# Performance work log

Measured on AMD Instinct MI355X. Metric: run time of the kernel, lower is better.

Reference implementation:

```python
import jax, jax.numpy as jnp
import numpy as np

B, T, D = 4, 2048, 1024
H = 16
HD = D // H  # 64


def setup_inputs() -> dict:
    key = jax.random.key(0)
    ks = jax.random.split(key, 5)
    scale = 0.02
    x = jax.random.normal(ks[0], (B, T, D), dtype=jnp.float32)
    W_qkv = jax.random.normal(ks[1], (D, 3 * D), dtype=jnp.float32) * scale
    b_qkv = jnp.zeros((3 * D,), dtype=jnp.float32)
    W_proj = jax.random.normal(ks[2], (D, D), dtype=jnp.float32) * scale
    b_proj = jnp.zeros((D,), dtype=jnp.float32)
    return {"x": x, "W_qkv": W_qkv, "b_qkv": b_qkv, "W_proj": W_proj, "b_proj": b_proj}


def reference(x, W_qkv, b_qkv, W_proj, b_proj):
    b, t, c = x.shape
    qkv = x @ W_qkv + b_qkv  # [b, t, 3c]
    q, k, v = jnp.split(qkv, 3, axis=-1)
    # [b, h, t, hd]
    q = q.reshape(b, t, H, HD).transpose(0, 2, 1, 3)
    k = k.reshape(b, t, H, HD).transpose(0, 2, 1, 3)
    v = v.reshape(b, t, H, HD).transpose(0, 2, 1, 3)
    att = jnp.einsum('bhqd,bhkd->bhqk', q, k) / jnp.sqrt(jnp.float32(HD))
    causal = jnp.tril(jnp.ones((t, t), dtype=bool))
    att = jnp.where(causal[None, None], att, jnp.float32(-jnp.inf))
    att = jax.nn.softmax(att, axis=-1)
    y = jnp.einsum('bhqk,bhkd->bhqd', att, v)
    y = y.transpose(0, 2, 1, 3).reshape(b, t, c)
    return y @ W_proj + b_proj
```

## Files before the change

kernel.cpp:

```cpp
#include <hip/hip_runtime.h>
#include <hip/hip_bf16.h>
#include <cmath>
#include <cstdint>
#include <type_traits>

#define B_ 4
#define T_ 2048
#define D_ 1024
#define H_ 16
#define HD_ 64
#define M_ (B_*T_)
#define NQKV_ 3072

#define SCALE_Q 0.18033688011112042f

typedef float f32x4 __attribute__((ext_vector_type(4)));
typedef float f32x16 __attribute__((ext_vector_type(16)));
typedef __bf16 bf16x8 __attribute__((ext_vector_type(8)));
typedef __bf16 bf16x4 __attribute__((ext_vector_type(4)));

#define MFMA16(a, b, c) __builtin_amdgcn_mfma_f32_16x16x32_bf16((a), (b), (c), 0, 0, 0)
#define MFMA32(a, b, c) __builtin_amdgcn_mfma_f32_32x32x16_bf16((a), (b), (c), 0, 0, 0)

#if defined(__has_builtin)
#if __has_builtin(__builtin_amdgcn_global_load_lds)
#define HAVE_GLDS 1
#endif
#if __has_builtin(__builtin_amdgcn_exp2f)
#define EXP2(x) __builtin_amdgcn_exp2f(x)
#endif
#endif
#ifndef EXP2
#define EXP2(x) exp2f(x)
#endif

#ifdef HAVE_GLDS
#define GLDS16(g, l) __builtin_amdgcn_global_load_lds( \
    (const __attribute__((address_space(1))) void*)(g), \
    (__attribute__((address_space(3))) void*)(l), 16, 0, 0)
#endif

__device__ inline uint32_t pack2bf(float a, float b) {
  union { __bf16 h[2]; uint32_t u; } x;
  x.h[0] = (__bf16)a; x.h[1] = (__bf16)b;
  return x.u;
}

__global__ __launch_bounds__(256) void k_cvt_bf16(const float4* __restrict__ in,
                                                  bf16x4* __restrict__ out, int n4) {
  int i = blockIdx.x * 256 + threadIdx.x;
  if (i >= n4) return;
  float4 v = in[i];
  bf16x4 o;
  o[0] = (__bf16)v.x; o[1] = (__bf16)v.y; o[2] = (__bf16)v.z; o[3] = (__bf16)v.w;
  out[i] = o;
}

__global__ __launch_bounds__(256) void k_transpose_cvt(const float* __restrict__ in,
                                                       __bf16* __restrict__ out,
                                                       int R, int C) {
  __shared__ float tile[64][65];
  int r0 = blockIdx.y * 64, c0 = blockIdx.x * 64;
#pragma unroll
  for (int i = 0; i < 16; ++i) {
    int e = threadIdx.x + i * 256;
    int lr = e >> 6, lc = e & 63;
    tile[lr][lc] = in[(size_t)(r0 + lr) * C + c0 + lc];
  }
  __syncthreads();
#pragma unroll
  for (int i = 0; i < 16; ++i) {
    int e = threadIdx.x + i * 256;
    int lc = e >> 6, lr = e & 63;
    out[(size_t)(c0 + lc) * R + r0 + lr] = (__bf16)tile[lr][lc];
  }
}

template <int MODE>
__global__ __launch_bounds__(256) void k_gemm(const __bf16* __restrict__ A,
                                              const __bf16* __restrict__ Bt,
                                              const float* __restrict__ bias,
                                              float* __restrict__ Cf,
                                              __bf16* __restrict__ Qb,
                                              __bf16* __restrict__ Kb,
                                              __bf16* __restrict__ Vtmp,
                                              int K, int N) {
  __shared__ __bf16 lA[128 * 32];
  __shared__ __bf16 lB[128 * 32];
  const int tid = threadIdx.x;
  const int lane = tid & 63, w = tid >> 6;
  const int wr = w >> 1, wc = w & 1;
  const int r15 = lane & 15, rg = lane >> 4;
  const int mb = blockIdx.y, nb = blockIdx.x;
  const int nk = K >> 5;

  const f32x4 zero = {0.f, 0.f, 0.f, 0.f};
  f32x4 acc[4][4];
#pragma unroll
  for (int m = 0; m < 4; ++m)
#pragma unroll
    for (int n = 0; n < 4; ++n) acc[m][n] = zero;

  const int c0 = tid, c1 = tid + 256;
  const int rowA0 = c0 >> 2, offA0 = (c0 & 3) * 8;
  const int rowA1 = c1 >> 2, offA1 = (c1 & 3) * 8;
  const __bf16* Ab = A + (size_t)(mb * 128) * K;
  const __bf16* Bb = Bt + (size_t)(nb * 128) * K;

  for (int kb = 0; kb < nk; ++kb) {
    __syncthreads();
#ifdef HAVE_GLDS
    GLDS16(Ab + (size_t)rowA0 * K + kb * 32 + offA0, &lA[c0 * 8]);
    GLDS16(Ab + (size_t)rowA1 * K + kb * 32 + offA1, &lA[c1 * 8]);
    GLDS16(Bb + (size_t)rowA0 * K + kb * 32 + offA0, &lB[c0 * 8]);
    GLDS16(Bb + (size_t)rowA1 * K + kb * 32 + offA1, &lB[c1 * 8]);
#else
    {
      bf16x8 ta0 = *(const bf16x8*)(Ab + (size_t)rowA0 * K + kb * 32 + offA0);
      bf16x8 ta1 = *(const bf16x8*)(Ab + (size_t)rowA1 * K + kb * 32 + offA1);
      bf16x8 tb0 = *(const bf16x8*)(Bb + (size_t)rowA0 * K + kb * 32 + offA0);
      bf16x8 tb1 = *(const bf16x8*)(Bb + (size_t)rowA1 * K + kb * 32 + offA1);
      *(bf16x8*)(&lA[c0 * 8]) = ta0;
      *(bf16x8*)(&lA[c1 * 8]) = ta1;
      *(bf16x8*)(&lB[c0 * 8]) = tb0;
      *(bf16x8*)(&lB[c1 * 8]) = tb1;
    }
#endif
    __syncthreads();
    bf16x8 af[4], bfr[4];
#pragma unroll
    for (int m = 0; m < 4; ++m)
      af[m] = *(const bf16x8*)(&lA[(wr * 64 + m * 16 + r15) * 32 + rg * 8]);
#pragma unroll
    for (int n = 0; n < 4; ++n)
      bfr[n] = *(const bf16x8*)(&lB[(wc * 64 + n * 16 + r15) * 32 + rg * 8]);
#pragma unroll
    for (int m = 0; m < 4; ++m)
#pragma unroll
      for (int n = 0; n < 4; ++n)
        acc[m][n] = MFMA16(af[m], bfr[n], acc[m][n]);
  }

  const int row0 = mb * 128 + wr * 64;
  const int col0 = nb * 128 + wc * 64;
#pragma unroll
  for (int m = 0; m < 4; ++m) {
#pragma unroll
    for (int n = 0; n < 4; ++n) {
#pragma unroll
      for (int j = 0; j < 4; ++j) {
        int r = row0 + m * 16 + rg * 4 + j;
        int c = col0 + n * 16 + r15;
        float v = acc[m][n][j] + bias[c];
        if (MODE == 0) {
          Cf[(size_t)r * N + c] = v;
        } else {
          int which = c >> 10, cc = c & 1023;
          int b = r >> 11, t = r & 2047;
          if (which == 0) {
            int hh = cc >> 6, hd = cc & 63;
            Qb[((size_t)(b * H_ + hh) * T_ + t) * HD_ + hd] = (__bf16)(v * SCALE_Q);
          } else if (which == 1) {
            int hh = cc >> 6, hd = cc & 63;
            Kb[((size_t)(b * H_ + hh) * T_ + t) * HD_ + hd] = (__bf16)v;
          } else {
            Vtmp[(size_t)r * D_ + cc] = (__bf16)v;
          }
        }
      }
    }
  }
}

__global__ __launch_bounds__(256) void k_vtrans(const __bf16* __restrict__ Vtmp,
                                                __bf16* __restrict__ Vt) {
  __shared__ __bf16 tile[64][72];
  const int bh = blockIdx.y;
  const int b = bh >> 4, h = bh & 15;
  const int t0 = blockIdx.x * 64;
  const int tid = threadIdx.x;
#pragma unroll
  for (int i = 0; i < 2; ++i) {
    int e = tid + i * 256;
    int tr = e >> 3, c8 = (e & 7) * 8;
    bf16x8 v = *(const bf16x8*)(Vtmp + (size_t)(b * T_ + t0 + tr) * D_ + h * HD_ + c8);
    *(bf16x8*)(&tile[tr][c8]) = v;
  }
  __syncthreads();
  const int hr = tid >> 2, tc0 = (tid & 3) * 16;
#pragma unroll
  for (int half = 0; half < 2; ++half) {
    bf16x8 o;
#pragma unroll
    for (int i = 0; i < 8; ++i) o[i] = tile[tc0 + half * 8 + i][hr];
    *(bf16x8*)(Vt + ((size_t)bh * HD_ + hr) * T_ + t0 + tc0 + half * 8) = o;
  }
}

__global__ __launch_bounds__(128) void k_attn(const __bf16* __restrict__ Qb,
                                              const __bf16* __restrict__ Kb,
                                              const __bf16* __restrict__ Vt,
                                              __bf16* __restrict__ Obuf) {
  __shared__ __bf16 lK[2][64 * 64];
  __shared__ __bf16 lV[2][64 * 64];
  const int tid = threadIdx.x;
  const int lane = tid & 63, w = tid >> 6;
  const int l31 = lane & 31, hi = lane >> 5;
  const int bh = blockIdx.y;
  const int b = bh >> 4, h = bh & 15;
  const __bf16* Qh = Qb + (size_t)bh * T_ * HD_;
  const __bf16* Kh = Kb + (size_t)bh * T_ * HD_;
  const __bf16* Vh = Vt + (size_t)bh * HD_ * T_;

  int sRow[4], sSw[4];
#pragma unroll
  for (int i = 0; i < 4; ++i) {
    int c = tid + i * 128;
    sRow[i] = c >> 3;
    sSw[i] = ((c & 7) ^ (sRow[i] & 7)) * 8;
  }

  auto STAGE = [&](int bufi, int kv0) {
#pragma unroll
    for (int i = 0; i < 4; ++i) {
      int c = tid + i * 128;
#ifdef HAVE_GLDS
      GLDS16(Kh + (size_t)(kv0 + sRow[i]) * HD_ + sSw[i], &lK[bufi][c * 8]);
      GLDS16(Vh + (size_t)sRow[i] * T_ + kv0 + sSw[i], &lV[bufi][c * 8]);
#else
      bf16x8 kv = *(const bf16x8*)(Kh + (size_t)(kv0 + sRow[i]) * HD_ + sSw[i]);
      bf16x8 vv = *(const bf16x8*)(Vh + (size_t)sRow[i] * T_ + kv0 + sSw[i]);
      *(bf16x8*)(&lK[bufi][c * 8]) = kv;
      *(bf16x8*)(&lV[bufi][c * 8]) = vv;
#endif
    }
  };

  int buf = 0;
  STAGE(0, 0);

  auto process_half = [&](int s, int nst, bool hasNext) {
    const int q0w = s * 64 + w * 32;
    bf16x8 qf[4];
#pragma unroll
    for (int ks = 0; ks < 4; ++ks)
      qf[ks] = *(const bf16x8*)(Qh + (size_t)(q0w + l31) * HD_ + ks * 16 + hi * 8);

    f32x16 o0, o1;
#pragma unroll
    for (int i = 0; i < 16; ++i) { o0[i] = 0.f; o1[i] = 0.f; }
    float mrun = -INFINITY, lrun = 0.f;

    for (int i = 0; i < nst; ++i) {
      const int kv0 = i * 64;
      if (i + 1 < nst) STAGE(buf ^ 1, (i + 1) * 64);
      else if (hasNext) STAGE(buf ^ 1, 0);

      if (kv0 <= q0w + 31) {
        const bool masked = (kv0 + 63) > q0w;
        bf16x8 kf[2][4];
#pragma unroll
        for (int seg = 0; seg < 2; ++seg)
#pragma unroll
          for (int ks = 0; ks < 4; ++ks)
            kf[seg][ks] = *(const bf16x8*)(&lK[buf][(seg * 32 + l31) * 64 +
                                                   (((ks * 2 + hi) ^ (l31 & 7)) * 8)]);
        f32x16 s0, s1;
#pragma unroll
        for (int r = 0; r < 16; ++r) { s0[r] = 0.f; s1[r] = 0.f; }
#pragma unroll
        for (int ks = 0; ks < 4; ++ks) s0 = MFMA32(kf[0][ks], qf[ks], s0);
#pragma unroll
        for (int ks = 0; ks < 4; ++ks) s1 = MFMA32(kf[1][ks], qf[ks], s1);

        if (masked) {
#pragma unroll
          for (int r = 0; r < 16; ++r) {
            int rr = (r & 3) + 8 * (r >> 2) + 4 * hi;
            if (kv0 + rr > q0w + l31) s0[r] = -INFINITY;
            if (kv0 + 32 + rr > q0w + l31) s1[r] = -INFINITY;
          }
        }
        float pmax = -INFINITY;
#pragma unroll
        for (int r = 0; r < 16; ++r) pmax = fmaxf(pmax, fmaxf(s0[r], s1[r]));
        pmax = fmaxf(pmax, __shfl_xor(pmax, 32, 64));

        if (__any(pmax > mrun + 8.0f)) {
          float mnew = fmaxf(mrun, pmax);
          float sc = EXP2(mrun - mnew);
#pragma unroll
          for (int r = 0; r < 16; ++r) {
            int rr = (r & 3) + 8 * (r >> 2) + 4 * hi;
            float scr = __shfl(sc, rr, 64);
            o0[r] *= scr; o1[r] *= scr;
          }
          lrun *= sc;
          mrun = mnew;
        }
        float rs = 0.f;
#pragma unroll
        for (int r = 0; r < 16; ++r) {
          s0[r] = EXP2(s0[r] - mrun); s1[r] = EXP2(s1[r] - mrun);
          rs += s0[r] + s1[r];
        }
        rs += __shfl_xor(rs, 32, 64);
        lrun += rs;

        bf16x8 vf[2][4];
#pragma unroll
        for (int dh = 0; dh < 2; ++dh)
#pragma unroll
          for (int ks = 0; ks < 4; ++ks)
            vf[dh][ks] = *(const bf16x8*)(&lV[buf][(dh * 32 + l31) * 64 +
                                                   (((ks * 2 + hi) ^ (l31 & 7)) * 8)]);

#pragma unroll
        for (int ks = 0; ks < 4; ++ks) {
          const f32x16& sv = (ks < 2) ? s0 : s1;
          const int off = (ks & 1) * 8;
          uint32_t w0 = pack2bf(sv[off + 0], sv[off + 1]);
          uint32_t w1 = pack2bf(sv[off + 2], sv[off + 3]);
          uint32_t w2 = pack2bf(sv[off + 4], sv[off + 5]);
          uint32_t w3 = pack2bf(sv[off + 6], sv[off + 7]);
          uint32_t sx = hi ? w0 : w2;
          uint32_t sy = hi ? w1 : w3;
          uint32_t px = (uint32_t)__shfl_xor((int)sx, 32, 64);
          uint32_t py = (uint32_t)__shfl_xor((int)sy, 32, 64);
          union { uint32_t u[4]; bf16x8 v; } pa;
          pa.u[0] = hi ? px : w0;
          pa.u[1] = hi ? py : w1;
          pa.u[2] = hi ? w2 : px;
          pa.u[3] = hi ? w3 : py;
          o0 = MFMA32(pa.v, vf[0][ks], o0);
          o1 = MFMA32(pa.v, vf[1][ks], o1);
        }
      }
      __syncthreads();
      buf ^= 1;
    }

#pragma unroll
    for (int r = 0; r < 16; ++r) {
      int rr = (r & 3) + 8 * (r >> 2) + 4 * hi;
      float inv = 1.0f / __shfl(lrun, rr, 64);
      int row = q0w + rr;
      __bf16* op = Obuf + (size_t)(b * T_ + row) * D_ + h * HD_ + l31;
      op[0]  = (__bf16)(o0[r] * inv);
      op[32] = (__bf16)(o1[r] * inv);
    }
  };

  const int sA = 31 - blockIdx.x;
  const int sB = blockIdx.x;
  __syncthreads();
  process_half(sA, sA + 1, true);
  process_half(sB, sB + 1, false);
}

extern "C" void kernel_launch(void* const* d_in, const int* in_sizes, int n_in,
                              void* d_out, int out_size, void* d_ws, size_t ws_size,
                              hipStream_t stream) {
  const float* x      = (const float*)d_in[0];
  const float* W_qkv  = (const float*)d_in[1];
  const float* b_qkv  = (const float*)d_in[2];
  const float* W_proj = (const float*)d_in[3];
  const float* b_proj = (const float*)d_in[4];
  float* out = (float*)d_out;

  char* ws = (char*)d_ws;
  size_t o = 0;
  __bf16* xb     = (__bf16*)(ws + o); o += (size_t)M_ * D_ * 2;
  __bf16* wqkvt  = (__bf16*)(ws + o); o += (size_t)NQKV_ * D_ * 2;
  __bf16* wprojt = (__bf16*)(ws + o); o += (size_t)D_ * D_ * 2;
  __bf16* Qb     = (__bf16*)(ws + o); o += (size_t)M_ * D_ * 2;
  __bf16* Kb     = (__bf16*)(ws + o); o += (size_t)M_ * D_ * 2;
  __bf16* Vtmp   = (__bf16*)(ws + o); o += (size_t)M_ * D_ * 2;
  __bf16* Vt     = (__bf16*)(ws + o); o += (size_t)M_ * D_ * 2;
  __bf16* Obuf   = (__bf16*)(ws + o); o += (size_t)M_ * D_ * 2;
  (void)ws_size; (void)in_sizes; (void)n_in; (void)out_size;

  k_cvt_bf16<<<(M_ * D_ / 4 + 255) / 256, 256, 0, stream>>>((const float4*)x, (bf16x4*)xb, M_ * D_ / 4);
  k_transpose_cvt<<<dim3(NQKV_ / 64, D_ / 64), 256, 0, stream>>>(W_qkv, wqkvt, D_, NQKV_);
  k_transpose_cvt<<<dim3(D_ / 64, D_ / 64), 256, 0, stream>>>(W_proj, wprojt, D_, D_);
  k_gemm<1><<<dim3(NQKV_ / 128, M_ / 128), 256, 0, stream>>>(xb, wqkvt, b_qkv, nullptr, Qb, Kb, Vtmp, D_, NQKV_);
  k_vtrans<<<dim3(T_ / 64, B_ * H_), 256, 0, stream>>>(Vtmp, Vt);
  k_attn<<<dim3(16, B_ * H_), 128, 0, stream>>>(Qb, Kb, Vt, Obuf);
  k_gemm<0><<<dim3(D_ / 128, M_ / 128), 256, 0, stream>>>(Obuf, wprojt, b_proj, out, nullptr, nullptr, nullptr, D_, D_);
}
```

Baseline: 219.2 us.

## Drop LDS staging in attention; load K/V straight from global per wave

Rewrites the attention kernel so each wave owns an independent 32-row query strip and loads K and V fragments directly from global memory into registers, with no shared-memory double buffering and no block barriers. Blocks grow to 256 threads with a flat 1024-block grid. The block-to-head mapping is interleaved and each wave's strip index is rotated within the block to spread causal work. Exp2 now uses inline v_exp_f32 asm. This removes LDS traffic and sync stalls but relies on L1/L2 to serve repeated K/V reads across waves, which may raise global load latency.

New measurement: 266.2 us. 21.5% more time.

```diff
diff --git a/kernel.cpp b/kernel.cpp
--- a/kernel.cpp
+++ b/kernel.cpp
@@ -2,7 +2,6 @@
 #include <hip/hip_bf16.h>
 #include <cmath>
 #include <cstdint>
-#include <type_traits>
 
 #define B_ 4
 #define T_ 2048
@@ -26,12 +25,6 @@
 #if __has_builtin(__builtin_amdgcn_global_load_lds)
 #define HAVE_GLDS 1
 #endif
-#if __has_builtin(__builtin_amdgcn_exp2f)
-#define EXP2(x) __builtin_amdgcn_exp2f(x)
-#endif
-#endif
-#ifndef EXP2
-#define EXP2(x) exp2f(x)
 #endif
 
 #ifdef HAVE_GLDS
@@ -39,6 +32,10 @@
     (const __attribute__((address_space(1))) void*)(g), \
     (__attribute__((address_space(3))) void*)(l), 16, 0, 0)
 #endif
+
+__device__ inline float hexp2(float x) {
+  float r; asm("v_exp_f32 %0, %1" : "=v"(r) : "v"(x)); return r;
+}
 
 __device__ inline uint32_t pack2bf(float a, float b) {
   union { __bf16 h[2]; uint32_t u; } x;
@@ -197,165 +194,130 @@
   }
 }
 
-__global__ __launch_bounds__(128) void k_attn(const __bf16* __restrict__ Qb,
-                                              const __bf16* __restrict__ Kb,
-                                              const __bf16* __restrict__ Vt,
-                                              __bf16* __restrict__ Obuf) {
-  __shared__ __bf16 lK[2][64 * 64];
-  __shared__ __bf16 lV[2][64 * 64];
+__global__ __launch_bounds__(256, 4) void k_attn(const __bf16* __restrict__ Qb,
+                                                 const __bf16* __restrict__ Kb,
+                                                 const __bf16* __restrict__ Vt,
+                                                 __bf16* __restrict__ Obuf) {
   const int tid = threadIdx.x;
   const int lane = tid & 63, w = tid >> 6;
   const int l31 = lane & 31, hi = lane >> 5;
-  const int bh = blockIdx.y;
+  const int bid = blockIdx.x;
+  const int bh = ((bid & 7) << 3) | ((bid >> 3) & 7);
+  const int s = (bid >> 6) + 16 * ((w + bid) & 3);
   const int b = bh >> 4, h = bh & 15;
+  const int q0w = s * 32;
   const __bf16* Qh = Qb + (size_t)bh * T_ * HD_;
   const __bf16* Kh = Kb + (size_t)bh * T_ * HD_;
   const __bf16* Vh = Vt + (size_t)bh * HD_ * T_;
 
-  int sRow[4], sSw[4];
-#pragma unroll
-  for (int i = 0; i < 4; ++i) {
-    int c = tid + i * 128;
-    sRow[i] = c >> 3;
-    sSw[i] = ((c & 7) ^ (sRow[i] & 7)) * 8;
-  }
-
-  auto STAGE = [&](int bufi, int kv0) {
-#pragma unroll
-    for (int i = 0; i < 4; ++i) {
-      int c = tid + i * 128;
-#ifdef HAVE_GLDS
-      GLDS16(Kh + (size_t)(kv0 + sRow[i]) * HD_ + sSw[i], &lK[bufi][c * 8]);
-      GLDS16(Vh + (size_t)sRow[i] * T_ + kv0 + sSw[i], &lV[bufi][c * 8]);
-#else
-      bf16x8 kv = *(const bf16x8*)(Kh + (size_t)(kv0 + sRow[i]) * HD_ + sSw[i]);
-      bf16x8 vv = *(const bf16x8*)(Vh + (size_t)sRow[i] * T_ + kv0 + sSw[i]);
-      *(bf16x8*)(&lK[bufi][c * 8]) = kv;
-      *(bf16x8*)(&lV[bufi][c * 8]) = vv;
-#endif
-    }
-  };
-
-  int buf = 0;
-  STAGE(0, 0);
-
-  auto process_half = [&](int s, int nst, bool hasNext) {
-    const int q0w = s * 64 + w * 32;
-    bf16x8 qf[4];
+  bf16x8 qf[4];
+#pragma unroll
+  for (int ks = 0; ks < 4; ++ks)
+    qf[ks] = *(const bf16x8*)(Qh + (size_t)(q0w + l31) * HD_ + ks * 16 + hi * 8);
+
+  f32x16 o0, o1;
+#pragma unroll
+  for (int i = 0; i < 16; ++i) { o0[i] = 0.f; o1[i] = 0.f; }
+  float mrun = -INFINITY, lrun = 0.f;
+
+  const int nst = ((q0w + 31) >> 6) + 1;
+  for (int i = 0; i < nst; ++i) {
+    const int kv0 = i * 64;
+    bf16x8 kf0[4], kf1[4];
 #pragma unroll
     for (int ks = 0; ks < 4; ++ks)
-      qf[ks] = *(const bf16x8*)(Qh + (size_t)(q0w + l31) * HD_ + ks * 16 + hi * 8);
-
-    f32x16 o0, o1;
-#pragma unroll
-    for (int i = 0; i < 16; ++i) { o0[i] = 0.f; o1[i] = 0.f; }
-    float mrun = -INFINITY, lrun = 0.f;
-
-    for (int i = 0; i < nst; ++i) {
-      const int kv0 = i * 64;
-      if (i + 1 < nst) STAGE(buf ^ 1, (i + 1) * 64);
-      else if (hasNext) STAGE(buf ^ 1, 0);
-
-      if (kv0 <= q0w + 31) {
-        const bool masked = (kv0 + 63) > q0w;
-        bf16x8 kf[2][4];
-#pragma unroll
-        for (int seg = 0; seg < 2; ++seg)
-#pragma unroll
-          for (int ks = 0; ks < 4; ++ks)
-            kf[seg][ks] = *(const bf16x8*)(&lK[buf][(seg * 32 + l31) * 64 +
-                                                   (((ks * 2 + hi) ^ (l31 & 7)) * 8)]);
-        f32x16 s0, s1;
-#pragma unroll
-        for (int r = 0; r < 16; ++r) { s0[r] = 0.f; s1[r] = 0.f; }
-#pragma unroll
-        for (int ks = 0; ks < 4; ++ks) s0 = MFMA32(kf[0][ks], qf[ks], s0);
-#pragma unroll
-        for (int ks = 0; ks < 4; ++ks) s1 = MFMA32(kf[1][ks], qf[ks], s1);
-
-        if (masked) {
-#pragma unroll
-          for (int r = 0; r < 16; ++r) {
-            int rr = (r & 3) + 8 * (r >> 2) + 4 * hi;
-            if (kv0 + rr > q0w + l31) s0[r] = -INFINITY;
-            if (kv0 + 32 + rr > q0w + l31) s1[r] = -INFINITY;
-          }
-        }
-        float pmax = -INFINITY;
-#pragma unroll
-        for (int r = 0; r < 16; ++r) pmax = fmaxf(pmax, fmaxf(s0[r], s1[r]));
-        pmax = fmaxf(pmax, __shfl_xor(pmax, 32, 64));
-
-        if (__any(pmax > mrun + 8.0f)) {
-          float mnew = fmaxf(mrun, pmax);
-          float sc = EXP2(mrun - mnew);
-#pragma unroll
-          for (int r = 0; r < 16; ++r) {
-            int rr = (r & 3) + 8 * (r >> 2) + 4 * hi;
-            float scr = __shfl(sc, rr, 64);
-            o0[r] *= scr; o1[r] *= scr;
-          }
-          lrun *= sc;
-          mrun = mnew;
-        }
-        float rs = 0.f;
-#pragma unroll
-        for (int r = 0; r < 16; ++r) {
-          s0[r] = EXP2(s0[r] - mrun); s1[r] = EXP2(s1[r] - mrun);
-          rs += s0[r] + s1[r];
-        }
-        rs += __shfl_xor(rs, 32, 64);
-        lrun += rs;
-
-        bf16x8 vf[2][4];
-#pragma unroll
-        for (int dh = 0; dh < 2; ++dh)
-#pragma unroll
-          for (int ks = 0; ks < 4; ++ks)
-            vf[dh][ks] = *(const bf16x8*)(&lV[buf][(dh * 32 + l31) * 64 +
-                                                   (((ks * 2 + hi) ^ (l31 & 7)) * 8)]);
-
-#pragma unroll
-        for (int ks = 0; ks < 4; ++ks) {
-          const f32x16& sv = (ks < 2) ? s0 : s1;
-          const int off = (ks & 1) * 8;
-          uint32_t w0 = pack2bf(sv[off + 0], sv[off + 1]);
-          uint32_t w1 = pack2bf(sv[off + 2], sv[off + 3]);
-          uint32_t w2 = pack2bf(sv[off + 4], sv[off + 5]);
-          uint32_t w3 = pack2bf(sv[off + 6], sv[off + 7]);
-          uint32_t sx = hi ? w0 : w2;
-          uint32_t sy = hi ? w1 : w3;
-          uint32_t px = (uint32_t)__shfl_xor((int)sx, 32, 64);
-          uint32_t py = (uint32_t)__shfl_xor((int)sy, 32, 64);
-          union { uint32_t u[4]; bf16x8 v; } pa;
-          pa.u[0] = hi ? px : w0;
-          pa.u[1] = hi ? py : w1;
-          pa.u[2] = hi ? w2 : px;
-          pa.u[3] = hi ? w3 : py;
-          o0 = MFMA32(pa.v, vf[0][ks], o0);
-          o1 = MFMA32(pa.v, vf[1][ks], o1);
-        }
+      kf0[ks] = *(const bf16x8*)(Kh + (size_t)(kv0 + l31) * HD_ + ks * 16 + hi * 8);
+#pragma unroll
+    for (int ks = 0; ks < 4; ++ks)
+      kf1[ks] = *(const bf16x8*)(Kh + (size_t)(kv0 + 32 + l31) * HD_ + ks * 16 + hi * 8);
+
+    f32x16 s0, s1;
+#pragma unroll
+    for (int r = 0; r < 16; ++r) { s0[r] = 0.f; s1[r] = 0.f; }
+#pragma unroll
+    for (int ks = 0; ks < 4; ++ks) s0 = MFMA32(kf0[ks], qf[ks], s0);
+#pragma unroll
+    for (int ks = 0; ks < 4; ++ks) s1 = MFMA32(kf1[ks], qf[ks], s1);
+
+    bf16x8 vf0[4];
+#pragma unroll
+    for (int ks = 0; ks < 4; ++ks)
+      vf0[ks] = *(const bf16x8*)(Vh + (size_t)(l31) * T_ + kv0 + ks * 16 + hi * 8);
+
+    if (kv0 + 63 > q0w) {
+#pragma unroll
+      for (int r = 0; r < 16; ++r) {
+        int rr = (r & 3) + 8 * (r >> 2) + 4 * hi;
+        if (kv0 + rr > q0w + l31) s0[r] = -INFINITY;
+        if (kv0 + 32 + rr > q0w + l31) s1[r] = -INFINITY;
       }
-      __syncthreads();
-      buf ^= 1;
-    }
-
+    }
+    float pmax = -INFINITY;
+#pragma unroll
+    for (int r = 0; r < 16; ++r) pmax = fmaxf(pmax, fmaxf(s0[r], s1[r]));
+    pmax = fmaxf(pmax, __shfl_xor(pmax, 32, 64));
+
+    if (__any(pmax > mrun + 8.0f)) {
+      float mnew = fmaxf(mrun, pmax);
+      float sc = hexp2(mrun - mnew);
+#pragma unroll
+      for (int r = 0; r < 16; ++r) {
+        int rr = (r & 3) + 8 * (r >> 2) + 4 * hi;
+        float scr = __shfl(sc, rr, 64);
+        o0[r] *= scr; o1[r] *= scr;
+      }
+      lrun *= sc;
+      mrun = mnew;
+    }
+    float rs = 0.f;
 #pragma unroll
     for (int r = 0; r < 16; ++r) {
-      int rr = (r & 3) + 8 * (r >> 2) + 4 * hi;
-      float inv = 1.0f / __shfl(lrun, rr, 64);
-      int row = q0w + rr;
-      __bf16* op = Obuf + (size_t)(b * T_ + row) * D_ + h * HD_ + l31;
-      op[0]  = (__bf16)(o0[r] * inv);
-      op[32] = (__bf16)(o1[r] * inv);
-    }
-  };
-
-  const int sA = 31 - blockIdx.x;
-  const int sB = blockIdx.x;
-  __syncthreads();
-  process_half(sA, sA + 1, true);
-  process_half(sB, sB + 1, false);
+      s0[r] = hexp2(s0[r] - mrun); s1[r] = hexp2(s1[r] - mrun);
+      rs += s0[r] + s1[r];
+    }
+    rs += __shfl_xor(rs, 32, 64);
+    lrun += rs;
+
+    bf16x8 pa[4];
+#pragma unroll
+    for (int ks = 0; ks < 4; ++ks) {
+      const f32x16& sv = (ks < 2) ? s0 : s1;
+      const int off = (ks & 1) * 8;
+      uint32_t w0 = pack2bf(sv[off + 0], sv[off + 1]);
+      uint32_t w1 = pack2bf(sv[off + 2], sv[off + 3]);
+      uint32_t w2 = pack2bf(sv[off + 4], sv[off + 5]);
+      uint32_t w3 = pack2bf(sv[off + 6], sv[off + 7]);
+      uint32_t sx = hi ? w0 : w2;
+      uint32_t sy = hi ? w1 : w3;
+      uint32_t px = (uint32_t)__shfl_xor((int)sx, 32, 64);
+      uint32_t py = (uint32_t)__shfl_xor((int)sy, 32, 64);
+      union { uint32_t u[4]; bf16x8 v; } pu;
+      pu.u[0] = hi ? px : w0;
+      pu.u[1] = hi ? py : w1;
+      pu.u[2] = hi ? w2 : px;
+      pu.u[3] = hi ? w3 : py;
+      pa[ks] = pu.v;
+    }
+
+#pragma unroll
+    for (int ks = 0; ks < 4; ++ks) o0 = MFMA32(pa[ks], vf0[ks], o0);
+    bf16x8 vf1[4];
+#pragma unroll
+    for (int ks = 0; ks < 4; ++ks)
+      vf1[ks] = *(const bf16x8*)(Vh + (size_t)(32 + l31) * T_ + kv0 + ks * 16 + hi * 8);
+#pragma unroll
+    for (int ks = 0; ks < 4; ++ks) o1 = MFMA32(pa[ks], vf1[ks], o1);
+  }
+
+#pragma unroll
+  for (int r = 0; r < 16; ++r) {
+    int rr = (r & 3) + 8 * (r >> 2) + 4 * hi;
+    float inv = 1.0f / __shfl(lrun, rr, 64);
+    int row = q0w + rr;
+    __bf16* op = Obuf + (size_t)(b * T_ + row) * D_ + h * HD_ + l31;
+    op[0]  = (__bf16)(o0[r] * inv);
+    op[32] = (__bf16)(o1[r] * inv);
+  }
 }
 
 extern "C" void kernel_launch(void* const* d_in, const int* in_sizes, int n_in,
@@ -385,6 +347,6 @@
   k_transpose_cvt<<<dim3(D_ / 64, D_ / 64), 256, 0, stream>>>(W_proj, wprojt, D_, D_);
   k_gemm<1><<<dim3(NQKV_ / 128, M_ / 128), 256, 0, stream>>>(xb, wqkvt, b_qkv, nullptr, Qb, Kb, Vtmp, D_, NQKV_);
   k_vtrans<<<dim3(T_ / 64, B_ * H_), 256, 0, stream>>>(Vtmp, Vt);
-  k_attn<<<dim3(16, B_ * H_), 128, 0, stream>>>(Qb, Kb, Vt, Obuf);
+  k_attn<<<dim3(1024), 256, 0, stream>>>(Qb, Kb, Vt, Obuf);
   k_gemm<0><<<dim3(D_ / 128, M_ / 128), 256, 0, stream>>>(Obuf, wprojt, b_proj, out, nullptr, nullptr, nullptr, D_, D_);
 }
```
